# Performance work log

Hardware: AMD Instinct MI355X
Metric: run time of the kernel (lower is better)

Reference implementation:

```python
import jax, jax.numpy as jnp
import numpy as np

B, NQ, NM, NHR, D, H, FF = 16, 100, 5440, 4096, 256, 8, 2048

def _ln(x, w, b):
    m = x.mean(-1, keepdims=True)
    v = ((x - m) ** 2).mean(-1, keepdims=True)
    return (x - m) * jax.lax.rsqrt(v + 1e-5) * w + b

def setup_inputs():
    key = jax.random.key(0)
    ks = iter(jax.random.split(key, 32))
    def rn(shape, s=1.0):
        return jax.random.normal(next(ks), shape, jnp.float32) * s
    return {
        'tgt': rn((B, NQ, D)),
        'memory': rn((B, NM, D)),
        'memory_hr': rn((B, NHR, D)),
        'prior_attn_bias': rn((B, NQ, NM)),
        'query_pos': rn((B, NQ, D)),
        'ln_cross_w': jnp.ones((D,)), 'ln_cross_b': jnp.zeros((D,)),
        'q_w': rn((D, D), 0.02), 'q_b': jnp.zeros((D,)),
        'k_w': rn((D, D), 0.02), 'k_b': jnp.zeros((D,)),
        'v_w': rn((D, D), 0.02), 'v_b': jnp.zeros((D,)),
        'out_w': rn((D, D), 0.02), 'out_b': jnp.zeros((D,)),
        'ln_self_w': jnp.ones((D,)), 'ln_self_b': jnp.zeros((D,)),
        'sa_in_w': rn((3 * D, D), 0.02), 'sa_in_b': jnp.zeros((3 * D,)),
        'sa_out_w': rn((D, D), 0.02), 'sa_out_b': jnp.zeros((D,)),
        'ln_ffn_w': jnp.ones((D,)), 'ln_ffn_b': jnp.zeros((D,)),
        'lin1_w': rn((FF, D), 0.02), 'lin1_b': jnp.zeros((FF,)),
        'lin2_w': rn((D, FF), 0.02), 'lin2_b': jnp.zeros((D,)),
        'me_w': rn((D, D), 0.02), 'me_b': jnp.zeros((D,)),
    }

def reference(tgt, memory, memory_hr, prior_attn_bias, query_pos,
              ln_cross_w, ln_cross_b, q_w, q_b, k_w, k_b, v_w, v_b,
              out_w, out_b, ln_self_w, ln_self_b, sa_in_w, sa_in_b,
              sa_out_w, sa_out_b, ln_ffn_w, ln_ffn_b, lin1_w, lin1_b,
              lin2_w, lin2_b, me_w, me_b):
    b, nq, d = tgt.shape
    nm = memory.shape[1]
    h = H
    dh = d // h
    scale = dh ** -0.5
    # ---- cross-attention with additive prior bias (eval mode: dropout = id) ----
    x = _ln(tgt, ln_cross_w, ln_cross_b)
    q = ((x + query_pos) @ q_w.T + q_b).reshape(b, nq, h, dh)
    k = (memory @ k_w.T + k_b).reshape(b, nm, h, dh)
    v = (memory @ v_w.T + v_b).reshape(b, nm, h, dh)
    attn = jnp.einsum('bqhd,bmhd->bhqm', q, k) * scale + prior_attn_bias[:, None]  # [b,h,nq,nm]
    a = jax.nn.softmax(attn, axis=-1)
    o = jnp.einsum('bhqm,bmhd->bqhd', a, v).reshape(b, nq, d)
    tgt = tgt + (o @ out_w.T + out_b)
    # ---- self-attention (torch nn.MultiheadAttention, batch_first, eval) ----
    z = _ln(tgt, ln_self_w, ln_self_b)
    zq = z + query_pos
    qs = (zq @ sa_in_w[:d].T + sa_in_b[:d]).reshape(b, nq, h, dh)
    ks = (zq @ sa_in_w[d:2 * d].T + sa_in_b[d:2 * d]).reshape(b, nq, h, dh)
    vs = (z @ sa_in_w[2 * d:].T + sa_in_b[2 * d:]).reshape(b, nq, h, dh)
    sattn = jax.nn.softmax(jnp.einsum('bqhd,bmhd->bhqm', qs, ks) * scale, axis=-1)
    so = jnp.einsum('bhqm,bmhd->bqhd', sattn, vs).reshape(b, nq, d)
    tgt = tgt + (so @ sa_out_w.T + sa_out_b)
    # ---- FFN ----
    y = _ln(tgt, ln_ffn_w, ln_ffn_b)
    y = jax.nn.gelu(y @ lin1_w.T + lin1_b, approximate=False) @ lin2_w.T + lin2_b
    tgt = tgt + y
    # ---- mask branch ----
    mask_logits = jnp.einsum('bqd,bmd->bqm', tgt @ me_w.T + me_b, memory_hr)
    return (tgt, mask_logits)
```

## Files before the change

kernel.cpp:

```cpp
#include <hip/hip_runtime.h>

typedef unsigned short u16;
typedef unsigned int u32;
typedef __bf16 bf16x8 __attribute__((ext_vector_type(8)));
typedef float f32x4 __attribute__((ext_vector_type(4)));

#define NCH 34
#define NSTEP 5

__device__ __forceinline__ u16 f2b(float f) {
  u32 u = __float_as_uint(f);
  u32 r = (u + 0x7fffu + ((u >> 16) & 1u)) >> 16;
  return (u16)r;
}
__device__ __forceinline__ float b2f(u16 h) {
  return __uint_as_float(((u32)h) << 16);
}
__device__ __forceinline__ bf16x8 zero8() {
  union { uint4 u; bf16x8 v; } z; z.u = make_uint4(0u, 0u, 0u, 0u); return z.v;
}
__device__ __forceinline__ u32 cvtpk(float lo, float hi) {
  u32 r;
  asm("v_cvt_pk_bf16_f32 %0, %1, %2" : "=v"(r) : "v"(lo), "v"(hi));
  return r;
}

struct Seg { const float* in; u16* out; int n4; };
struct PrepArgs {
  Seg seg[7];
  const float *k_w, *v_w, *k_b, *v_b, *pbias;
  u16 *Wf;
  uint4 *biasT4;
  float *kvB;
};

__global__ __launch_bounds__(256)
void prep_kernel(PrepArgs a)
{
  __shared__ float S[100][34];
  const int bx = blockIdx.x, tid = threadIdx.x;
  if (bx < 1472) {
    int bxr = bx;
#pragma unroll
    for (int k = 0; k < 7; ++k) {
      const int nb = a.seg[k].n4 >> 8;
      if (bxr < nb) {
        const int i = bxr * 256 + tid;
        const float4 f = *(const float4*)(a.seg[k].in + (size_t)i * 4);
        uint2 pk; pk.x = cvtpk(f.x, f.y); pk.y = cvtpk(f.z, f.w);
        *(uint2*)(a.seg[k].out + (size_t)i * 4) = pk;
        return;
      }
      bxr -= nb;
    }
    return;
  } else if (bx < 1536) {
    const int i = bx - 1472, gI = i >> 3, ks = i & 7;
    const int nt = tid >> 6, lane = tid & 63, lr = lane & 15, g = lane >> 4;
    const float* src = (gI < 4 ? a.k_w + (size_t)(gI * 64 + nt * 16 + lr) * 256
                               : a.v_w + (size_t)((gI - 4) * 64 + nt * 16 + lr) * 256)
                       + ks * 32 + g * 8;
    const float4 f0 = *(const float4*)src;
    const float4 f1 = *(const float4*)(src + 4);
    uint4 pk;
    pk.x = cvtpk(f0.x, f0.y); pk.y = cvtpk(f0.z, f0.w);
    pk.z = cvtpk(f1.x, f1.y); pk.w = cvtpk(f1.z, f1.w);
    *(uint4*)(a.Wf + (size_t)((gI * 8 + ks) * 4 + nt) * 512 + lane * 8) = pk;
  } else if (bx < 1538) {
    const int i = (bx - 1536) * 256 + tid;
    a.kvB[i] = (i < 256) ? a.k_b[i] : a.v_b[i - 256];
  } else {
    const int bt = bx - 1538;
    const int b = bt / 170, sg = bt - b * 170;
    const int m0 = sg * 32;
    for (int idx = tid; idx < 800; idx += 256) {
      const int q = idx >> 3, seg = idx & 7;
      const float4 v = *(const float4*)(a.pbias + (size_t)(b * 100 + q) * 5440 + m0 + seg * 4);
      S[q][seg * 4 + 0] = v.x; S[q][seg * 4 + 1] = v.y;
      S[q][seg * 4 + 2] = v.z; S[q][seg * 4 + 3] = v.w;
    }
    __syncthreads();
    for (int idx = tid; idx < 448; idx += 256) {
      const int mt = idx >> 6, lane = idx & 63;
      const int lr = lane & 15, g = lane >> 4;
      const int q0 = mt * 16 + g * 4;
      u16 h[8];
#pragma unroll
      for (int r = 0; r < 4; ++r) {
        const int q = q0 + r;
        h[r]     = (q < 100) ? f2b(S[q][lr])      : (u16)0;
        h[4 + r] = (q < 100) ? f2b(S[q][16 + lr]) : (u16)0;
      }
      uint4 pk;
      pk.x = (u32)h[0] | ((u32)h[1] << 16);
      pk.y = (u32)h[2] | ((u32)h[3] << 16);
      pk.z = (u32)h[4] | ((u32)h[5] << 16);
      pk.w = (u32)h[6] | ((u32)h[7] << 16);
      a.biasT4[((size_t)bt * 7 + mt) * 64 + lane] = pk;
    }
  }
}

template<int ROWS>
__device__ __forceinline__ void ln_stage(const float* __restrict__ x, int row0,
    const float* __restrict__ w, const float* __restrict__ b,
    const float* __restrict__ pos, u16* As)
{
  const int tid = threadIdx.x, lane = tid & 63, wid = tid >> 6;
  const float4 wv = *(const float4*)(w + lane * 4);
  const float4 bv = *(const float4*)(b + lane * 4);
#pragma unroll
  for (int rr = 0; rr < ROWS / 4; ++rr) {
    const int rl = wid * (ROWS / 4) + rr;
    const size_t o = (size_t)(row0 + rl) * 256 + lane * 4;
    const float4 v = *(const float4*)(x + o);
    float s = v.x + v.y + v.z + v.w;
#pragma unroll
    for (int m = 1; m < 64; m <<= 1) s += __shfl_xor(s, m);
    const float mean = s * (1.f / 256.f);
    const float d0 = v.x - mean, d1 = v.y - mean, d2 = v.z - mean, d3 = v.w - mean;
    float ss = d0 * d0 + d1 * d1 + d2 * d2 + d3 * d3;
#pragma unroll
    for (int m = 1; m < 64; m <<= 1) ss += __shfl_xor(ss, m);
    const float rs = rsqrtf(ss * (1.f / 256.f) + 1e-5f);
    float y0 = d0 * rs * wv.x + bv.x;
    float y1 = d1 * rs * wv.y + bv.y;
    float y2 = d2 * rs * wv.z + bv.z;
    float y3 = d3 * rs * wv.w + bv.w;
    if (pos) {
      const float4 pv = *(const float4*)(pos + o);
      y0 += pv.x; y1 += pv.y; y2 += pv.z; y3 += pv.w;
    }
    uint2 pk; pk.x = cvtpk(y0, y1); pk.y = cvtpk(y2, y3);
    const int byte = (rl * 512 + lane * 8) ^ ((rl & 7) << 4);
    *(uint2*)((char*)As + byte) = pk;
  }
}

__device__ __forceinline__ void gemm16x128(const u16* As, const u16* __restrict__ W,
                                           u16 (*Ws)[40], f32x4 acc[2])
{
  const int tid = threadIdx.x, lane = tid & 63, wid = tid >> 6;
  const int g = lane >> 4, lr = lane & 15;
  for (int k0 = 0; k0 < 256; k0 += 32) {
    for (int cid = tid; cid < 512; cid += 256) {
      const int r = cid >> 2, cg = (cid & 3) * 8;
      *(uint4*)&Ws[r][cg] = *(const uint4*)(W + (size_t)r * 256 + k0 + cg);
    }
    __syncthreads();
    const int abyte = (lr * 512 + k0 * 2 + g * 16) ^ ((lr & 7) << 4);
    const bf16x8 af = *(const bf16x8*)((const char*)As + abyte);
#pragma unroll
    for (int nt = 0; nt < 2; ++nt) {
      const bf16x8 bfr = *(const bf16x8*)&Ws[wid * 32 + nt * 16 + lr][g * 8];
      acc[nt] = __builtin_amdgcn_mfma_f32_16x16x32_bf16(af, bfr, acc[nt], 0, 0, 0);
    }
    __syncthreads();
  }
}

__global__ __launch_bounds__(256)
void qproj_kernel(const float* __restrict__ x, const float* __restrict__ lnw,
                  const float* __restrict__ lnb, const float* __restrict__ pos,
                  const u16* __restrict__ W, const float* __restrict__ bias,
                  u16* __restrict__ out, float scale)
{
  __shared__ u16 As[16 * 256];
  __shared__ u16 Ws[128][40];
  const int tid = threadIdx.x, lane = tid & 63, wid = tid >> 6;
  const int g = lane >> 4, lr = lane & 15;
  const int row0 = blockIdx.x * 16, n0 = blockIdx.y * 128;
  ln_stage<16>(x, row0, lnw, lnb, pos, As);
  f32x4 acc[2] = {};
  gemm16x128(As, W + (size_t)n0 * 256, Ws, acc);
#pragma unroll
  for (int nt = 0; nt < 2; ++nt) {
    const int col = n0 + wid * 32 + nt * 16 + lr;
    const float bv = bias[col];
#pragma unroll
    for (int r = 0; r < 4; ++r) {
      const int row = row0 + g * 4 + r;
      out[(size_t)row * 256 + col] = f2b((acc[nt][r] + bv) * scale);
    }
  }
}

__global__ __launch_bounds__(256)
void sain_kernel(const float* __restrict__ x, const float* __restrict__ lnw,
                 const float* __restrict__ lnb, const float* __restrict__ pos,
                 const u16* __restrict__ W, const float* __restrict__ bias,
                 float* __restrict__ qkb, float* __restrict__ vsb)
{
  __shared__ u16 As[16 * 256];
  __shared__ u16 Ws[128][40];
  const int tid = threadIdx.x, lane = tid & 63, wid = tid >> 6;
  const int g = lane >> 4, lr = lane & 15;
  const int row0 = blockIdx.x * 16, y = blockIdx.y;
  ln_stage<16>(x, row0, lnw, lnb, (y < 4) ? pos : nullptr, As);
  f32x4 acc[2] = {};
  gemm16x128(As, W + (size_t)y * 128 * 256, Ws, acc);
#pragma unroll
  for (int nt = 0; nt < 2; ++nt) {
    const int cl = wid * 32 + nt * 16 + lr;
    const float bv = bias[y * 128 + cl];
#pragma unroll
    for (int r = 0; r < 4; ++r) {
      const int row = row0 + g * 4 + r;
      const float v = acc[nt][r] + bv;
      if (y < 4) qkb[(size_t)row * 512 + y * 128 + cl] = v;
      else       vsb[(size_t)row * 256 + (y - 4) * 128 + cl] = v;
    }
  }
}

__global__ __launch_bounds__(256)
void ffn1_kernel(const float* __restrict__ x, const float* __restrict__ lnw,
                 const float* __restrict__ lnb, const u16* __restrict__ W,
                 const float* __restrict__ bias, u16* __restrict__ out)
{
  __shared__ u16 As[64 * 256];
  __shared__ u16 Ws[256][40];
  const int tid = threadIdx.x, lane = tid & 63, wid = tid >> 6;
  const int g = lane >> 4, lr = lane & 15;
  const int row0 = blockIdx.x * 64, n0 = blockIdx.y * 256;
  ln_stage<64>(x, row0, lnw, lnb, nullptr, As);
  f32x4 acc[16] = {};
  for (int k0 = 0; k0 < 256; k0 += 32) {
    for (int cid = tid; cid < 1024; cid += 256) {
      const int r = cid >> 2, cg = (cid & 3) * 8;
      *(uint4*)&Ws[r][cg] = *(const uint4*)(W + (size_t)(n0 + r) * 256 + k0 + cg);
    }
    __syncthreads();
    const int arow = wid * 16 + lr;
    const int abyte = (arow * 512 + k0 * 2 + g * 16) ^ ((arow & 7) << 4);
    const bf16x8 af = *(const bf16x8*)((const char*)As + abyte);
#pragma unroll
    for (int nt = 0; nt < 16; ++nt) {
      const bf16x8 bfr = *(const bf16x8*)&Ws[nt * 16 + lr][g * 8];
      acc[nt] = __builtin_amdgcn_mfma_f32_16x16x32_bf16(af, bfr, acc[nt], 0, 0, 0);
    }
    __syncthreads();
  }
#pragma unroll
  for (int nt = 0; nt < 16; ++nt) {
    const int col = n0 + nt * 16 + lr;
    const float bv = bias[col];
#pragma unroll
    for (int r = 0; r < 4; ++r) {
      const int row = row0 + wid * 16 + g * 4 + r;
      float v = acc[nt][r] + bv;
      v = 0.5f * v * (1.f + erff(v * 0.70710678118654752f));
      out[(size_t)row * 2048 + col] = f2b(v);
    }
  }
}

template<int BM, int BN, int WM, int WN, int GELU_, int RES_, int OF32, int OBF>
__global__ __launch_bounds__(256)
void gemm_kernel(const u16* __restrict__ Ap, const u16* __restrict__ W,
                 const float* __restrict__ bias, const float* __restrict__ res,
                 float* __restrict__ Cf, u16* __restrict__ Cb,
                 int M, int N, int K, float scale)
{
  constexpr int WROWS = BM / WM;
  constexpr int WCOLS = BN / WN;
  constexpr int MT = WROWS / 16;
  constexpr int NT = WCOLS / 16;
  static_assert(WM * WN == 4, "4 waves");
  __shared__ u16 As[BM][40];
  __shared__ u16 Ws[BN][40];
  const int tid = threadIdx.x, lane = tid & 63, wid = tid >> 6;
  const int g = lane >> 4, lr = lane & 15;
  const int m0 = blockIdx.x * BM, n0 = blockIdx.y * BN;
  const int wm = wid / WN, wn = wid % WN;
  f32x4 acc[MT][NT] = {};
  for (int k0 = 0; k0 < K; k0 += 32) {
    for (int cid = tid; cid < BM * 4; cid += 256) {
      int r = cid >> 2, cg = (cid & 3) * 8;
      *(uint4*)&As[r][cg] = *(const uint4*)(Ap + (size_t)(m0 + r) * K + k0 + cg);
    }
    for (int cid = tid; cid < BN * 4; cid += 256) {
      int r = cid >> 2, cg = (cid & 3) * 8;
      *(uint4*)&Ws[r][cg] = *(const uint4*)(W + (size_t)(n0 + r) * K + k0 + cg);
    }
    __syncthreads();
    bf16x8 af[MT], bfr[NT];
#pragma unroll
    for (int mt = 0; mt < MT; ++mt) af[mt] = *(const bf16x8*)&As[wm * WROWS + mt * 16 + lr][g * 8];
#pragma unroll
    for (int nt = 0; nt < NT; ++nt) bfr[nt] = *(const bf16x8*)&Ws[wn * WCOLS + nt * 16 + lr][g * 8];
#pragma unroll
    for (int mt = 0; mt < MT; ++mt)
#pragma unroll
      for (int nt = 0; nt < NT; ++nt)
        acc[mt][nt] = __builtin_amdgcn_mfma_f32_16x16x32_bf16(af[mt], bfr[nt], acc[mt][nt], 0, 0, 0);
    __syncthreads();
  }
#pragma unroll
  for (int mt = 0; mt < MT; ++mt)
#pragma unroll
    for (int nt = 0; nt < NT; ++nt) {
      const int col = n0 + wn * WCOLS + nt * 16 + lr;
      const float bv = bias[col];
#pragma unroll
      for (int r = 0; r < 4; ++r) {
        const int row = m0 + wm * WROWS + mt * 16 + g * 4 + r;
        float v = (acc[mt][nt][r] + bv) * scale;
        if constexpr (GELU_) v = 0.5f * v * (1.f + erff(v * 0.70710678118654752f));
        if constexpr (RES_) v += res[(size_t)row * N + col];
        if constexpr (OF32) Cf[(size_t)row * N + col] = v;
        if constexpr (OBF) Cb[(size_t)row * N + col] = f2b(v);
      }
    }
}

__global__ __launch_bounds__(512, 4)
void kv_gemm_kernel(const float* __restrict__ A, const u16* __restrict__ Wf,
                    const float* __restrict__ biasKV,
                    u16* __restrict__ Kb, u16* __restrict__ Vt)
{
  __shared__ u16 As[64 * 256];
  __shared__ u16 Vs[256 * 64];
  const int tid = threadIdx.x, lane = tid & 63, wid = tid >> 6;
  const int g = lane >> 4, lr = lane & 15;
  const int bidx = blockIdx.x / 85, t = blockIdx.x - bidx * 85;
  const int row0 = blockIdx.x * 64;

  for (int ch = tid; ch < 2048; ch += 512) {
    const int r = ch >> 5, c8 = (ch & 31) * 8;
    const float* ap = A + (size_t)(row0 + r) * 256 + c8;
    const float4 f0 = *(const float4*)ap;
    const float4 f1 = *(const float4*)(ap + 4);
    uint4 pk;
    pk.x = cvtpk(f0.x, f0.y);
    pk.y = cvtpk(f0.z, f0.w);
    pk.z = cvtpk(f1.x, f1.y);
    pk.w = cvtpk(f1.z, f1.w);
    const int byte = r * 512 + c8 * 2;
    *(uint4*)((char*)As + (byte ^ ((r & 7) << 4))) = pk;
  }
  __syncthreads();

  const u16* wbase = Wf + (size_t)wid * 8 * 4 * 512 + lane * 8;
  f32x4 acc[4][4] = {};
#pragma unroll 2
  for (int ks = 0; ks < 8; ++ks) {
    bf16x8 bfv[4], af[4];
#pragma unroll
    for (int nt = 0; nt < 4; ++nt)
      bfv[nt] = *(const bf16x8*)(wbase + (ks * 4 + nt) * 512);
#pragma unroll
    for (int mt = 0; mt < 4; ++mt) {
      const int r = mt * 16 + lr;
      const int byte = r * 512 + ks * 64 + g * 16;
      af[mt] = *(const bf16x8*)((const char*)As + (byte ^ ((r & 7) << 4)));
    }
#pragma unroll
    for (int mt = 0; mt < 4; ++mt)
#pragma unroll
      for (int nt = 0; nt < 4; ++nt)
        acc[mt][nt] = __builtin_amdgcn_mfma_f32_16x16x32_bf16(af[mt], bfv[nt], acc[mt][nt], 0, 0, 0);
  }

  const int isV = wid >> 2;
  if (isV) {
#pragma unroll
    for (int nt = 0; nt < 4; ++nt) {
      const int col = (wid - 4) * 64 + nt * 16 + lr;
      const float bv = biasKV[256 + col];
#pragma unroll
      for (int a = 0; a < 2; ++a)
#pragma unroll
        for (int r = 0; r < 4; ++r) {
          const u32 val = cvtpk(acc[2 * a][nt][r] + bv, acc[2 * a + 1][nt][r] + bv);
          const int byte = (col * 128 + a * 64 + g * 16 + r * 4) ^ ((col & 7) << 4);
          *(u32*)((char*)Vs + byte) = val;
        }
    }
  }
  __syncthreads();

  if (!isV) {
#pragma unroll
    for (int nt = 0; nt < 4; ++nt) {
      const int col = wid * 64 + nt * 16 + lr;
      const float bv = biasKV[col];
#pragma unroll
      for (int mt = 0; mt < 4; ++mt)
#pragma unroll
        for (int r = 0; r < 4; r += 2) {
          const u32 pk = cvtpk(acc[mt][nt][r] + bv, acc[mt][nt][r + 1] + bv);
          const int rowA = mt * 16 + g * 4 + r;
          const int rowB = rowA + 1;
          *(u16*)((char*)As + ((rowA * 512 + col * 2) ^ ((rowA & 7) << 4))) = (u16)pk;
          *(u16*)((char*)As + ((rowB * 512 + col * 2) ^ ((rowB & 7) << 4))) = (u16)(pk >> 16);
        }
    }
  } else {
    const size_t vbase = (size_t)bidx * 256 * 5440 + (size_t)t * 64;
    const int t2 = tid - 256;
#pragma unroll
    for (int p = 0; p < 8; ++p) {
      const int idx = p * 256 + t2;
      const int col = idx >> 3, chunk = idx & 7;
      const int lbyte = col * 128 + ((chunk * 16) ^ ((col & 7) << 4));
      const uint4 v = *(const uint4*)((const char*)Vs + lbyte);
      *(uint4*)(Vt + vbase + (size_t)col * 5440 + chunk * 8) = v;
    }
  }
  __syncthreads();
#pragma unroll
  for (int p = 0; p < 4; ++p) {
    const int idx = p * 512 + tid;
    const int row = idx >> 5, c16 = idx & 31;
    const int lbyte = row * 512 + ((c16 * 16) ^ ((row & 7) << 4));
    const uint4 v = *(const uint4*)((const char*)As + lbyte);
    *(uint4*)(Kb + (size_t)(row0 + row) * 256 + c16 * 8) = v;
  }
}

__global__ __launch_bounds__(256, 3)
void cross_attn_kernel(const u16* __restrict__ Q, const u16* __restrict__ Kb,
                       const u16* __restrict__ Vt, const uint4* __restrict__ biasT4,
                       u32* __restrict__ Opp, float* __restrict__ ML)
{
  __shared__ u32 P32[4][112][20];
  const int tid = threadIdx.x, lane = tid & 63, wid = tid >> 6;
  const int g = lane >> 4, lr = lane & 15;
  const int b = blockIdx.y, c = blockIdx.x;
  const int head = blockIdx.z * 4 + wid;
  const int m_base = c * (5440 / NCH);
  const f32x4 zf = {0.f, 0.f, 0.f, 0.f};

  bf16x8 qf[7];
#pragma unroll
  for (int mt = 0; mt < 7; ++mt) {
    int qr = mt * 16 + lr;
    qf[mt] = (qr < 100) ? *(const bf16x8*)&Q[(size_t)(b * 100 + qr) * 256 + head * 32 + g * 8]
                        : zero8();
  }
  float Mst[7];
  f32x4 Lp[7];
  f32x4 Oa[7][2];
#pragma unroll
  for (int mt = 0; mt < 7; ++mt) { Mst[mt] = -1e30f; Lp[mt] = zf; Oa[mt][0] = zf; Oa[mt][1] = zf; }

  for (int s = 0; s < NSTEP; ++s) {
    const int m0 = m_base + s * 32;
    const uint4* bb4 = biasT4 + ((size_t)(b * 170 + c * NSTEP + s) * 7) * 64 + lane;
    const bf16x8 kf0 = *(const bf16x8*)&Kb[(size_t)(b * 5440 + m0 + lr) * 256 + head * 32 + g * 8];
    const bf16x8 kf1 = *(const bf16x8*)&Kb[(size_t)(b * 5440 + m0 + 16 + lr) * 256 + head * 32 + g * 8];
    const size_t vrow = ((size_t)(b * 8 + head) * 32 + lr) * 5440 + m0 + g * 8;
    const bf16x8 vf0 = *(const bf16x8*)&Vt[vrow];
    const bf16x8 vf1 = *(const bf16x8*)&Vt[vrow + 16 * 5440];
#pragma unroll
    for (int mt = 0; mt < 7; ++mt) {
      const uint4 bq = bb4[mt * 64];
      __builtin_amdgcn_s_setprio(1);
      f32x4 s0 = __builtin_amdgcn_mfma_f32_16x16x32_bf16(qf[mt], kf0, zf, 0, 0, 0);
      f32x4 s1 = __builtin_amdgcn_mfma_f32_16x16x32_bf16(qf[mt], kf1, zf, 0, 0, 0);
      __builtin_amdgcn_s_setprio(0);
      s0[0] += b2f((u16)bq.x);      s0[1] += b2f((u16)(bq.x >> 16));
      s0[2] += b2f((u16)bq.y);      s0[3] += b2f((u16)(bq.y >> 16));
      s1[0] += b2f((u16)bq.z);      s1[1] += b2f((u16)(bq.z >> 16));
      s1[2] += b2f((u16)bq.w);      s1[3] += b2f((u16)(bq.w >> 16));
      float mx = fmaxf(fmaxf(fmaxf(s0[0], s0[1]), fmaxf(s0[2], s0[3])),
                       fmaxf(fmaxf(s1[0], s1[1]), fmaxf(s1[2], s1[3])));
#pragma unroll
      for (int d = 1; d < 16; d <<= 1) mx = fmaxf(mx, __shfl_xor(mx, d, 16));
      const float newM = fmaxf(Mst[mt], mx);
      const float al = __expf(Mst[mt] - newM);
      Mst[mt] = newM;
      f32x4 p0, p1;
#pragma unroll
      for (int r = 0; r < 4; ++r) {
        p0[r] = __expf(s0[r] - newM);
        p1[r] = __expf(s1[r] - newM);
      }
      Lp[mt] = Lp[mt] * al + (p0 + p1);
      Oa[mt][0] *= al;
      Oa[mt][1] *= al;
#pragma unroll
      for (int r = 0; r < 4; ++r)
        P32[wid][mt * 16 + g * 4 + r][lr] = cvtpk(p0[r], p1[r]);
    }
    __builtin_amdgcn_s_setprio(1);
#pragma unroll
    for (int mt = 0; mt < 7; ++mt) {
      const bf16x8 pa = *(const bf16x8*)&P32[wid][mt * 16 + lr][g * 4];
      Oa[mt][0] = __builtin_amdgcn_mfma_f32_16x16x32_bf16(pa, vf0, Oa[mt][0], 0, 0, 0);
      Oa[mt][1] = __builtin_amdgcn_mfma_f32_16x16x32_bf16(pa, vf1, Oa[mt][1], 0, 0, 0);
    }
    __builtin_amdgcn_s_setprio(0);
  }
  const int bh = b * 8 + head;
#pragma unroll
  for (int mt = 0; mt < 7; ++mt)
#pragma unroll
    for (int r = 0; r < 4; ++r) {
      const int qr = mt * 16 + g * 4 + r;
      if (qr < 100) {
        float L = Lp[mt][r];
#pragma unroll
        for (int d = 1; d < 16; d <<= 1) L += __shfl_xor(L, d, 16);
        const size_t rb = (size_t)(bh * NCH + c) * 100 + qr;
        Opp[rb * 16 + lr] = cvtpk(Oa[mt][0][r], Oa[mt][1][r]);
        if (lr == 0) { ML[rb * 2] = Mst[mt]; ML[rb * 2 + 1] = L; }
      }
    }
}

__global__ __launch_bounds__(256)
void reduce_attn_kernel(const u32* __restrict__ Opp, const float* __restrict__ ML,
                        u16* __restrict__ outb)
{
  const int row = blockIdx.x;
  const int b = row / 100, q = row % 100;
  const int h = threadIdx.x >> 5, d = threadIdx.x & 31;
  const int bh = b * 8 + h;
  const int hi = d >> 4, dl = d & 15;
  float gm = -1e30f;
  for (int c = 0; c < NCH; ++c) gm = fmaxf(gm, ML[((size_t)(bh * NCH + c) * 100 + q) * 2]);
  float l = 0.f, o = 0.f;
  for (int c = 0; c < NCH; ++c) {
    const size_t rb = (size_t)(bh * NCH + c) * 100 + q;
    const float w = __expf(ML[rb * 2] - gm);
    l += ML[rb * 2 + 1] * w;
    const u32 pv = Opp[rb * 16 + dl];
    o += b2f((u16)(hi ? (pv >> 16) : pv)) * w;
  }
  outb[(size_t)row * 256 + h * 32 + d] = f2b(o / l);
}

__global__ __launch_bounds__(128)
void self_attn_kernel(const float* __restrict__ qk, const float* __restrict__ vs,
                      u16* __restrict__ so)
{
  __shared__ u16 kk[100][36];
  __shared__ u16 vv[100][36];
  __shared__ float S[100][101];
  const int b = blockIdx.x >> 3, h = blockIdx.x & 7;
  const int t = threadIdx.x;
  for (int e = t; e < 3200; e += 128) {
    const int r = e >> 5, cq = e & 31;
    kk[r][cq] = f2b(qk[(size_t)(b * 100 + r) * 512 + 256 + h * 32 + cq]);
    vv[r][cq] = f2b(vs[(size_t)(b * 100 + r) * 256 + h * 32 + cq]);
  }
  __syncthreads();
  if (t < 100) {
    float qr_[32];
#pragma unroll
    for (int cq = 0; cq < 32; ++cq) qr_[cq] = qk[(size_t)(b * 100 + t) * 512 + h * 32 + cq];
    for (int m = 0; m < 100; ++m) {
      float dp = 0.f;
#pragma unroll
      for (int cq = 0; cq < 32; ++cq) dp += qr_[cq] * b2f(kk[m][cq]);
      S[t][m] = dp * 0.17677669529663687f;
    }
    float mx = -1e30f;
    for (int m = 0; m < 100; ++m) mx = fmaxf(mx, S[t][m]);
    float sum = 0.f;
    for (int m = 0; m < 100; ++m) { const float p = __expf(S[t][m] - mx); S[t][m] = p; sum += p; }
    const float inv = 1.f / sum;
    float o[32];
#pragma unroll
    for (int cq = 0; cq < 32; ++cq) o[cq] = 0.f;
    for (int m = 0; m < 100; ++m) {
      const float p = S[t][m];
#pragma unroll
      for (int cq = 0; cq < 32; ++cq) o[cq] += p * b2f(vv[m][cq]);
    }
#pragma unroll
    for (int cq = 0; cq < 32; ++cq)
      so[(size_t)(b * 100 + t) * 256 + h * 32 + cq] = f2b(o[cq] * inv);
  }
}

__global__ __launch_bounds__(256)
void mask_gemm_kernel(const u16* __restrict__ tm, const float* __restrict__ hr,
                      float* __restrict__ out)
{
  __shared__ u16 As[112][40];
  __shared__ u16 Bs[64][40];
  const int tid = threadIdx.x, lane = tid & 63, wid = tid >> 6;
  const int g = lane >> 4, lr = lane & 15;
  const int b = blockIdx.y, n0 = blockIdx.x * 64;
  f32x4 acc[7] = {};
  for (int k0 = 0; k0 < 256; k0 += 32) {
    for (int cid = tid; cid < 448; cid += 256) {
      const int r = cid >> 2, cg = (cid & 3) * 8;
      uint4 val = {0u, 0u, 0u, 0u};
      if (r < 100) val = *(const uint4*)&tm[(size_t)(b * 100 + r) * 256 + k0 + cg];
      *(uint4*)&As[r][cg] = val;
    }
    {
      const int r = tid >> 2, cg = (tid & 3) * 8;
      const float* hp = hr + (size_t)(b * 4096 + n0 + r) * 256 + k0 + cg;
      float4 f0 = *(const float4*)hp;
      float4 f1 = *(const float4*)(hp + 4);
      uint4 pk;
      pk.x = cvtpk(f0.x, f0.y); pk.y = cvtpk(f0.z, f0.w);
      pk.z = cvtpk(f1.x, f1.y); pk.w = cvtpk(f1.z, f1.w);
      *(uint4*)&Bs[r][cg] = pk;
    }
    __syncthreads();
    const bf16x8 bfr = *(const bf16x8*)&Bs[wid * 16 + lr][g * 8];
#pragma unroll
    for (int mt = 0; mt < 7; ++mt) {
      const bf16x8 af = *(const bf16x8*)&As[mt * 16 + lr][g * 8];
      acc[mt] = __builtin_amdgcn_mfma_f32_16x16x32_bf16(af, bfr, acc[mt], 0, 0, 0);
    }
    __syncthreads();
  }
#pragma unroll
  for (int mt = 0; mt < 7; ++mt)
#pragma unroll
    for (int r = 0; r < 4; ++r) {
      const int qr = mt * 16 + g * 4 + r;
      if (qr < 100)
        out[(size_t)(b * 100 + qr) * 4096 + n0 + wid * 16 + lr] = acc[mt][r];
    }
}

extern "C" void kernel_launch(void* const* d_in, const int* in_sizes, int n_in,
                              void* d_out, int out_size, void* d_ws, size_t ws_size,
                              hipStream_t stream)
{
  (void)in_sizes; (void)n_in; (void)out_size; (void)ws_size;
  const float* tgt      = (const float*)d_in[0];
  const float* memory   = (const float*)d_in[1];
  const float* memhr    = (const float*)d_in[2];
  const float* pbias    = (const float*)d_in[3];
  const float* qpos     = (const float*)d_in[4];
  const float* lncw     = (const float*)d_in[5];
  const float* lncb     = (const float*)d_in[6];
  const float* q_w      = (const float*)d_in[7];
  const float* q_b      = (const float*)d_in[8];
  const float* k_w      = (const float*)d_in[9];
  const float* k_b      = (const float*)d_in[10];
  const float* v_w      = (const float*)d_in[11];
  const float* v_b      = (const float*)d_in[12];
  const float* out_w    = (const float*)d_in[13];
  const float* out_b    = (const float*)d_in[14];
  const float* lnsw     = (const float*)d_in[15];
  const float* lnsb     = (const float*)d_in[16];
  const float* sa_in_w  = (const float*)d_in[17];
  const float* sa_in_b  = (const float*)d_in[18];
  const float* sa_out_w = (const float*)d_in[19];
  const float* sa_out_b = (const float*)d_in[20];
  const float* lnfw     = (const float*)d_in[21];
  const float* lnfb     = (const float*)d_in[22];
  const float* l1w      = (const float*)d_in[23];
  const float* l1b      = (const float*)d_in[24];
  const float* l2w      = (const float*)d_in[25];
  const float* l2b      = (const float*)d_in[26];
  const float* me_w     = (const float*)d_in[27];
  const float* me_b     = (const float*)d_in[28];
  float* outf = (float*)d_out;

  char* ws = (char*)d_ws;
  size_t off = 0;
  auto alloc = [&](size_t bytes) -> void* {
    void* p = ws + off;
    off = (off + bytes + 255) & ~(size_t)255;
    return p;
  };
  u16*   Wf    = (u16*)alloc((size_t)131072 * 2);
  u16*   qW    = (u16*)alloc((size_t)65536 * 2);
  u16*   outW  = (u16*)alloc((size_t)65536 * 2);
  u16*   saW   = (u16*)alloc((size_t)196608 * 2);
  u16*   saoW  = (u16*)alloc((size_t)65536 * 2);
  u16*   l1W   = (u16*)alloc((size_t)524288 * 2);
  u16*   l2W   = (u16*)alloc((size_t)524288 * 2);
  u16*   meW   = (u16*)alloc((size_t)65536 * 2);
  float* kvB   = (float*)alloc((size_t)512 * 4);
  uint4* biasT4= (uint4*)alloc((size_t)16 * 170 * 7 * 64 * 16);
  u16*   Qb    = (u16*)alloc((size_t)409600 * 2);
  u16*   Kb    = (u16*)alloc((size_t)22282240 * 2);
  u16*   Vt    = (u16*)alloc((size_t)22282240 * 2);
  u32*   Opp   = (u32*)alloc((size_t)(128 * NCH * 100 * 16) * 4);
  float* MLp   = (float*)alloc((size_t)(128 * NCH * 100 * 2) * 4);
  u16*   attno = (u16*)alloc((size_t)409600 * 2);
  float* tgt1  = (float*)alloc((size_t)409600 * 4);
  float* qkb   = (float*)alloc((size_t)819200 * 4);
  float* vsb   = (float*)alloc((size_t)409600 * 4);
  u16*   sob   = (u16*)alloc((size_t)409600 * 2);
  float* tgt2  = (float*)alloc((size_t)409600 * 4);
  u16*   hb    = (u16*)alloc((size_t)3276800 * 2);
  u16*   t3b   = (u16*)alloc((size_t)409600 * 2);
  u16*   tmb   = (u16*)alloc((size_t)409600 * 2);

  const float SCALE = 0.17677669529663687f;

  PrepArgs pa;
  pa.seg[0] = {q_w,      qW,   16384};
  pa.seg[1] = {out_w,    outW, 16384};
  pa.seg[2] = {sa_in_w,  saW,  49152};
  pa.seg[3] = {sa_out_w, saoW, 16384};
  pa.seg[4] = {l1w,      l1W,  131072};
  pa.seg[5] = {l2w,      l2W,  131072};
  pa.seg[6] = {me_w,     meW,  16384};
  pa.k_w = k_w; pa.v_w = v_w; pa.k_b = k_b; pa.v_b = v_b; pa.pbias = pbias;
  pa.Wf = Wf; pa.biasT4 = biasT4; pa.kvB = kvB;
  prep_kernel<<<4258, 256, 0, stream>>>(pa);

  qproj_kernel<<<dim3(100, 2), 256, 0, stream>>>(tgt, lncw, lncb, qpos, qW, q_b, Qb, SCALE);
  kv_gemm_kernel<<<dim3(1360), 512, 0, stream>>>(memory, Wf, kvB, Kb, Vt);
  cross_attn_kernel<<<dim3(NCH, 16, 2), 256, 0, stream>>>(Qb, Kb, Vt, biasT4, Opp, MLp);
  reduce_attn_kernel<<<1600, 256, 0, stream>>>(Opp, MLp, attno);
  gemm_kernel<16, 128, 1, 4, 0, 1, 1, 0><<<dim3(100, 2), 256, 0, stream>>>(
      attno, outW, out_b, tgt, tgt1, nullptr, 1600, 256, 256, 1.f);

  sain_kernel<<<dim3(100, 6), 256, 0, stream>>>(tgt1, lnsw, lnsb, qpos, saW, sa_in_b, qkb, vsb);
  self_attn_kernel<<<128, 128, 0, stream>>>(qkb, vsb, sob);
  gemm_kernel<16, 128, 1, 4, 0, 1, 1, 0><<<dim3(100, 2), 256, 0, stream>>>(
      sob, saoW, sa_out_b, tgt1, tgt2, nullptr, 1600, 256, 256, 1.f);

  ffn1_kernel<<<dim3(25, 8), 256, 0, stream>>>(tgt2, lnfw, lnfb, l1W, l1b, hb);
  gemm_kernel<16, 128, 1, 4, 0, 1, 1, 1><<<dim3(100, 2), 256, 0, stream>>>(
      hb, l2W, l2b, tgt2, outf, t3b, 1600, 256, 2048, 1.f);

  gemm_kernel<16, 128, 1, 4, 0, 0, 0, 1><<<dim3(100, 2), 256, 0, stream>>>(
      t3b, meW, me_b, nullptr, nullptr, tmb, 1600, 256, 256, 1.f);
  mask_gemm_kernel<<<dim3(64, 16), 256, 0, stream>>>(tmb, memhr, outf + 409600);
}
```

Measured before the change: 336.2 us.

## Switch cross-attention to 32x32x16 MFMA with transposed scores, drop LDS P staging

Rewrites the cross-attention inner loop to compute S^T = K·Q^T with 32x32x16 bf16 MFMAs, so each lane owns one query column and the softmax max/sum need only a single cross-half shuffle. Probabilities then feed the PV MFMA straight from registers as the B operand, which removes the per-step LDS round trip for P. The prior-bias layout, the V tile layout in the KV GEMM, the partial-output layout and the reduce kernel are all reworked to match the new register mapping. In exchange, query rows are padded from 112 to 128, which adds wasted MFMA work and larger partial buffers, and register pressure goes up.

```diff
diff --git a/kernel.cpp b/kernel.cpp
--- a/kernel.cpp
+++ b/kernel.cpp
@@ -4,6 +4,7 @@
 typedef unsigned int u32;
 typedef __bf16 bf16x8 __attribute__((ext_vector_type(8)));
 typedef float f32x4 __attribute__((ext_vector_type(4)));
+typedef float f32x16 __attribute__((ext_vector_type(16)));
 
 #define NCH 34
 #define NSTEP 5
@@ -30,7 +31,7 @@
   Seg seg[7];
   const float *k_w, *v_w, *k_b, *v_b, *pbias;
   u16 *Wf;
-  uint4 *biasT4;
+  uint4 *biasT5;
   float *kvB;
 };
 
@@ -80,23 +81,25 @@
       S[q][seg * 4 + 2] = v.z; S[q][seg * 4 + 3] = v.w;
     }
     __syncthreads();
-    for (int idx = tid; idx < 448; idx += 256) {
-      const int mt = idx >> 6, lane = idx & 63;
-      const int lr = lane & 15, g = lane >> 4;
-      const int q0 = mt * 16 + g * 4;
-      u16 h[8];
-#pragma unroll
-      for (int r = 0; r < 4; ++r) {
-        const int q = q0 + r;
-        h[r]     = (q < 100) ? f2b(S[q][lr])      : (u16)0;
-        h[4 + r] = (q < 100) ? f2b(S[q][16 + lr]) : (u16)0;
+#pragma unroll
+    for (int pass = 0; pass < 2; ++pass) {
+      const int idx = pass * 256 + tid;
+      const int qb = idx >> 7, r2 = idx & 127;
+      const int half = r2 >> 6, lane = r2 & 63;
+      const int q = qb * 32 + (lane & 31), hh = lane >> 5;
+      u16 hv[8];
+#pragma unroll
+      for (int i = 0; i < 8; ++i) {
+        const int reg = half * 8 + i;
+        const int m = (reg & 3) + 8 * (reg >> 2) + 4 * hh;
+        hv[i] = (q < 100) ? f2b(S[q][m]) : (u16)0;
       }
       uint4 pk;
-      pk.x = (u32)h[0] | ((u32)h[1] << 16);
-      pk.y = (u32)h[2] | ((u32)h[3] << 16);
-      pk.z = (u32)h[4] | ((u32)h[5] << 16);
-      pk.w = (u32)h[6] | ((u32)h[7] << 16);
-      a.biasT4[((size_t)bt * 7 + mt) * 64 + lane] = pk;
+      pk.x = (u32)hv[0] | ((u32)hv[1] << 16);
+      pk.y = (u32)hv[2] | ((u32)hv[3] << 16);
+      pk.z = (u32)hv[4] | ((u32)hv[5] << 16);
+      pk.w = (u32)hv[6] | ((u32)hv[7] << 16);
+      a.biasT5[((size_t)(bt * 4 + qb)) * 128 + half * 64 + lane] = pk;
     }
   }
 }
@@ -369,13 +372,15 @@
       const int col = (wid - 4) * 64 + nt * 16 + lr;
       const float bv = biasKV[256 + col];
 #pragma unroll
-      for (int a = 0; a < 2; ++a)
-#pragma unroll
-        for (int r = 0; r < 4; ++r) {
-          const u32 val = cvtpk(acc[2 * a][nt][r] + bv, acc[2 * a + 1][nt][r] + bv);
-          const int byte = (col * 128 + a * 64 + g * 16 + r * 4) ^ ((col & 7) << 4);
+      for (int mt = 0; mt < 4; ++mt) {
+        const int slot = (mt >> 1) * 32 + 16 * (mt & 1) + 8 * (g & 1) + 4 * (g >> 1);
+#pragma unroll
+        for (int r = 0; r < 4; r += 2) {
+          const u32 val = cvtpk(acc[mt][nt][r] + bv, acc[mt][nt][r + 1] + bv);
+          const int byte = (col * 128 + (slot + r) * 2) ^ ((col & 7) << 4);
           *(u32*)((char*)Vs + byte) = val;
         }
+      }
     }
   }
   __syncthreads();
@@ -421,93 +426,102 @@
 
 __global__ __launch_bounds__(256, 3)
 void cross_attn_kernel(const u16* __restrict__ Q, const u16* __restrict__ Kb,
-                       const u16* __restrict__ Vt, const uint4* __restrict__ biasT4,
+                       const u16* __restrict__ Vt, const uint4* __restrict__ biasT5,
                        u32* __restrict__ Opp, float* __restrict__ ML)
 {
-  __shared__ u32 P32[4][112][20];
-  const int tid = threadIdx.x, lane = tid & 63, wid = tid >> 6;
-  const int g = lane >> 4, lr = lane & 15;
+  const int tid = threadIdx.x, lane = tid & 63, wid = tid >> 6;
+  const int ql = lane & 31, hh = lane >> 5;
   const int b = blockIdx.y, c = blockIdx.x;
   const int head = blockIdx.z * 4 + wid;
   const int m_base = c * (5440 / NCH);
-  const f32x4 zf = {0.f, 0.f, 0.f, 0.f};
-
-  bf16x8 qf[7];
-#pragma unroll
-  for (int mt = 0; mt < 7; ++mt) {
-    int qr = mt * 16 + lr;
-    qf[mt] = (qr < 100) ? *(const bf16x8*)&Q[(size_t)(b * 100 + qr) * 256 + head * 32 + g * 8]
-                        : zero8();
-  }
-  float Mst[7];
-  f32x4 Lp[7];
-  f32x4 Oa[7][2];
-#pragma unroll
-  for (int mt = 0; mt < 7; ++mt) { Mst[mt] = -1e30f; Lp[mt] = zf; Oa[mt][0] = zf; Oa[mt][1] = zf; }
+
+  bf16x8 qf[4][2];
+#pragma unroll
+  for (int qb = 0; qb < 4; ++qb) {
+    const int q = qb * 32 + ql;
+#pragma unroll
+    for (int hf = 0; hf < 2; ++hf)
+      qf[qb][hf] = (q < 100)
+        ? *(const bf16x8*)&Q[(size_t)(b * 100 + q) * 256 + head * 32 + hf * 16 + hh * 8]
+        : zero8();
+  }
+  float M[4], L[4];
+  f32x16 O[4];
+#pragma unroll
+  for (int qb = 0; qb < 4; ++qb) {
+    M[qb] = -1e30f; L[qb] = 0.f;
+#pragma unroll
+    for (int i = 0; i < 16; ++i) O[qb][i] = 0.f;
+  }
 
   for (int s = 0; s < NSTEP; ++s) {
     const int m0 = m_base + s * 32;
-    const uint4* bb4 = biasT4 + ((size_t)(b * 170 + c * NSTEP + s) * 7) * 64 + lane;
-    const bf16x8 kf0 = *(const bf16x8*)&Kb[(size_t)(b * 5440 + m0 + lr) * 256 + head * 32 + g * 8];
-    const bf16x8 kf1 = *(const bf16x8*)&Kb[(size_t)(b * 5440 + m0 + 16 + lr) * 256 + head * 32 + g * 8];
-    const size_t vrow = ((size_t)(b * 8 + head) * 32 + lr) * 5440 + m0 + g * 8;
-    const bf16x8 vf0 = *(const bf16x8*)&Vt[vrow];
-    const bf16x8 vf1 = *(const bf16x8*)&Vt[vrow + 16 * 5440];
-#pragma unroll
-    for (int mt = 0; mt < 7; ++mt) {
-      const uint4 bq = bb4[mt * 64];
+    const u16* kp = &Kb[(size_t)(b * 5440 + m0 + ql) * 256 + head * 32 + hh * 8];
+    const bf16x8 kf0 = *(const bf16x8*)kp;
+    const bf16x8 kf1 = *(const bf16x8*)(kp + 16);
+    const u16* vp = &Vt[((size_t)(b * 8 + head) * 32 + ql) * 5440 + m0 + hh * 8];
+    const bf16x8 vf0 = *(const bf16x8*)vp;
+    const bf16x8 vf1 = *(const bf16x8*)(vp + 16);
+    const uint4* bb = biasT5 + ((size_t)(b * 170 + c * NSTEP + s) * 4) * 128 + lane;
+#pragma unroll
+    for (int qb = 0; qb < 4; ++qb) {
+      const uint4 b0 = bb[qb * 128];
+      const uint4 b1 = bb[qb * 128 + 64];
+      f32x16 Sv = {};
       __builtin_amdgcn_s_setprio(1);
-      f32x4 s0 = __builtin_amdgcn_mfma_f32_16x16x32_bf16(qf[mt], kf0, zf, 0, 0, 0);
-      f32x4 s1 = __builtin_amdgcn_mfma_f32_16x16x32_bf16(qf[mt], kf1, zf, 0, 0, 0);
+      Sv = __builtin_amdgcn_mfma_f32_32x32x16_bf16(kf0, qf[qb][0], Sv, 0, 0, 0);
+      Sv = __builtin_amdgcn_mfma_f32_32x32x16_bf16(kf1, qf[qb][1], Sv, 0, 0, 0);
       __builtin_amdgcn_s_setprio(0);
-      s0[0] += b2f((u16)bq.x);      s0[1] += b2f((u16)(bq.x >> 16));
-      s0[2] += b2f((u16)bq.y);      s0[3] += b2f((u16)(bq.y >> 16));
-      s1[0] += b2f((u16)bq.z);      s1[1] += b2f((u16)(bq.z >> 16));
-      s1[2] += b2f((u16)bq.w);      s1[3] += b2f((u16)(bq.w >> 16));
-      float mx = fmaxf(fmaxf(fmaxf(s0[0], s0[1]), fmaxf(s0[2], s0[3])),
-                       fmaxf(fmaxf(s1[0], s1[1]), fmaxf(s1[2], s1[3])));
-#pragma unroll
-      for (int d = 1; d < 16; d <<= 1) mx = fmaxf(mx, __shfl_xor(mx, d, 16));
-      const float newM = fmaxf(Mst[mt], mx);
-      const float al = __expf(Mst[mt] - newM);
-      Mst[mt] = newM;
-      f32x4 p0, p1;
-#pragma unroll
-      for (int r = 0; r < 4; ++r) {
-        p0[r] = __expf(s0[r] - newM);
-        p1[r] = __expf(s1[r] - newM);
+      const u32 bw[8] = {b0.x, b0.y, b0.z, b0.w, b1.x, b1.y, b1.z, b1.w};
+#pragma unroll
+      for (int i = 0; i < 8; ++i) {
+        Sv[2 * i]     += b2f((u16)bw[i]);
+        Sv[2 * i + 1] += b2f((u16)(bw[i] >> 16));
       }
-      Lp[mt] = Lp[mt] * al + (p0 + p1);
-      Oa[mt][0] *= al;
-      Oa[mt][1] *= al;
-#pragma unroll
-      for (int r = 0; r < 4; ++r)
-        P32[wid][mt * 16 + g * 4 + r][lr] = cvtpk(p0[r], p1[r]);
-    }
-    __builtin_amdgcn_s_setprio(1);
-#pragma unroll
-    for (int mt = 0; mt < 7; ++mt) {
-      const bf16x8 pa = *(const bf16x8*)&P32[wid][mt * 16 + lr][g * 4];
-      Oa[mt][0] = __builtin_amdgcn_mfma_f32_16x16x32_bf16(pa, vf0, Oa[mt][0], 0, 0, 0);
-      Oa[mt][1] = __builtin_amdgcn_mfma_f32_16x16x32_bf16(pa, vf1, Oa[mt][1], 0, 0, 0);
-    }
-    __builtin_amdgcn_s_setprio(0);
+      float t8[8];
+#pragma unroll
+      for (int i = 0; i < 8; ++i) t8[i] = fmaxf(Sv[2 * i], Sv[2 * i + 1]);
+      float t4a = fmaxf(fmaxf(t8[0], t8[1]), fmaxf(t8[2], t8[3]));
+      float t4b = fmaxf(fmaxf(t8[4], t8[5]), fmaxf(t8[6], t8[7]));
+      float mx = fmaxf(t4a, t4b);
+      mx = fmaxf(mx, __shfl_xor(mx, 32));
+      const float newM = fmaxf(M[qb], mx);
+      const float al = __expf(M[qb] - newM);
+      M[qb] = newM;
+      float p[16];
+#pragma unroll
+      for (int i = 0; i < 16; ++i) p[i] = __expf(Sv[i] - newM);
+      float s8[8];
+#pragma unroll
+      for (int i = 0; i < 8; ++i) s8[i] = p[2 * i] + p[2 * i + 1];
+      const float sum = ((s8[0] + s8[1]) + (s8[2] + s8[3])) + ((s8[4] + s8[5]) + (s8[6] + s8[7]));
+      L[qb] = L[qb] * al + sum;
+#pragma unroll
+      for (int i = 0; i < 16; ++i) O[qb][i] *= al;
+      union { uint4 u; bf16x8 v; } pb0, pb1;
+      pb0.u.x = cvtpk(p[0], p[1]);   pb0.u.y = cvtpk(p[2], p[3]);
+      pb0.u.z = cvtpk(p[4], p[5]);   pb0.u.w = cvtpk(p[6], p[7]);
+      pb1.u.x = cvtpk(p[8], p[9]);   pb1.u.y = cvtpk(p[10], p[11]);
+      pb1.u.z = cvtpk(p[12], p[13]); pb1.u.w = cvtpk(p[14], p[15]);
+      __builtin_amdgcn_s_setprio(1);
+      O[qb] = __builtin_amdgcn_mfma_f32_32x32x16_bf16(vf0, pb0.v, O[qb], 0, 0, 0);
+      O[qb] = __builtin_amdgcn_mfma_f32_32x32x16_bf16(vf1, pb1.v, O[qb], 0, 0, 0);
+      __builtin_amdgcn_s_setprio(0);
+    }
   }
   const int bh = b * 8 + head;
 #pragma unroll
-  for (int mt = 0; mt < 7; ++mt)
-#pragma unroll
-    for (int r = 0; r < 4; ++r) {
-      const int qr = mt * 16 + g * 4 + r;
-      if (qr < 100) {
-        float L = Lp[mt][r];
-#pragma unroll
-        for (int d = 1; d < 16; d <<= 1) L += __shfl_xor(L, d, 16);
-        const size_t rb = (size_t)(bh * NCH + c) * 100 + qr;
-        Opp[rb * 16 + lr] = cvtpk(Oa[mt][0][r], Oa[mt][1][r]);
-        if (lr == 0) { ML[rb * 2] = Mst[mt]; ML[rb * 2 + 1] = L; }
-      }
-    }
+  for (int qb = 0; qb < 4; ++qb) {
+    const int q = qb * 32 + ql;
+    const float Lt = L[qb] + __shfl_xor(L[qb], 32);
+    if (q < 100) {
+      const size_t rb = (size_t)(bh * NCH + c) * 128 + q;
+#pragma unroll
+      for (int i = 0; i < 8; ++i)
+        Opp[rb * 16 + hh * 8 + i] = cvtpk(O[qb][2 * i], O[qb][2 * i + 1]);
+      if (hh == 0) { ML[rb * 2] = M[qb]; ML[rb * 2 + 1] = Lt; }
+    }
+  }
 }
 
 __global__ __launch_bounds__(256)
@@ -518,16 +532,18 @@
   const int b = row / 100, q = row % 100;
   const int h = threadIdx.x >> 5, d = threadIdx.x & 31;
   const int bh = b * 8 + h;
-  const int hi = d >> 4, dl = d & 15;
+  const int reg = (d & 3) + 4 * (d >> 3);
+  const int slot = ((d >> 2) & 1) * 8 + (reg >> 1);
+  const int half = reg & 1;
   float gm = -1e30f;
-  for (int c = 0; c < NCH; ++c) gm = fmaxf(gm, ML[((size_t)(bh * NCH + c) * 100 + q) * 2]);
+  for (int c = 0; c < NCH; ++c) gm = fmaxf(gm, ML[((size_t)(bh * NCH + c) * 128 + q) * 2]);
   float l = 0.f, o = 0.f;
   for (int c = 0; c < NCH; ++c) {
-    const size_t rb = (size_t)(bh * NCH + c) * 100 + q;
+    const size_t rb = (size_t)(bh * NCH + c) * 128 + q;
     const float w = __expf(ML[rb * 2] - gm);
     l += ML[rb * 2 + 1] * w;
-    const u32 pv = Opp[rb * 16 + dl];
-    o += b2f((u16)(hi ? (pv >> 16) : pv)) * w;
+    const u32 pv = Opp[rb * 16 + slot];
+    o += b2f((u16)(half ? (pv >> 16) : pv)) * w;
   }
   outb[(size_t)row * 256 + h * 32 + d] = f2b(o / l);
 }
@@ -674,12 +690,12 @@
   u16*   l2W   = (u16*)alloc((size_t)524288 * 2);
   u16*   meW   = (u16*)alloc((size_t)65536 * 2);
   float* kvB   = (float*)alloc((size_t)512 * 4);
-  uint4* biasT4= (uint4*)alloc((size_t)16 * 170 * 7 * 64 * 16);
+  uint4* biasT5= (uint4*)alloc((size_t)16 * 170 * 4 * 128 * 16);
   u16*   Qb    = (u16*)alloc((size_t)409600 * 2);
   u16*   Kb    = (u16*)alloc((size_t)22282240 * 2);
   u16*   Vt    = (u16*)alloc((size_t)22282240 * 2);
-  u32*   Opp   = (u32*)alloc((size_t)(128 * NCH * 100 * 16) * 4);
-  float* MLp   = (float*)alloc((size_t)(128 * NCH * 100 * 2) * 4);
+  u32*   Opp   = (u32*)alloc((size_t)(128 * NCH * 128 * 16) * 4);
+  float* MLp   = (float*)alloc((size_t)(128 * NCH * 128 * 2) * 4);
   u16*   attno = (u16*)alloc((size_t)409600 * 2);
   float* tgt1  = (float*)alloc((size_t)409600 * 4);
   float* qkb   = (float*)alloc((size_t)819200 * 4);
@@ -701,12 +717,12 @@
   pa.seg[5] = {l2w,      l2W,  131072};
   pa.seg[6] = {me_w,     meW,  16384};
   pa.k_w = k_w; pa.v_w = v_w; pa.k_b = k_b; pa.v_b = v_b; pa.pbias = pbias;
-  pa.Wf = Wf; pa.biasT4 = biasT4; pa.kvB = kvB;
+  pa.Wf = Wf; pa.biasT5 = biasT5; pa.kvB = kvB;
   prep_kernel<<<4258, 256, 0, stream>>>(pa);
 
   qproj_kernel<<<dim3(100, 2), 256, 0, stream>>>(tgt, lncw, lncb, qpos, qW, q_b, Qb, SCALE);
   kv_gemm_kernel<<<dim3(1360), 512, 0, stream>>>(memory, Wf, kvB, Kb, Vt);
-  cross_attn_kernel<<<dim3(NCH, 16, 2), 256, 0, stream>>>(Qb, Kb, Vt, biasT4, Opp, MLp);
+  cross_attn_kernel<<<dim3(NCH, 16, 2), 256, 0, stream>>>(Qb, Kb, Vt, biasT5, Opp, MLp);
   reduce_attn_kernel<<<1600, 256, 0, stream>>>(Opp, MLp, attno);
   gemm_kernel<16, 128, 1, 4, 0, 1, 1, 0><<<dim3(100, 2), 256, 0, stream>>>(
       attno, outW, out_b, tgt, tgt1, nullptr, 1600, 256, 256, 1.f);
```

Result: no change. 336.7 us (+0.1%).
